# Kernel optimization log

Measured on AMD Instinct MI355X. Metric: run time of the kernel, lower is better.

The kernel has to match this reference:

```python
import jax, jax.numpy as jnp
import numpy as np

N = 100000   # nodes
E = 1600000  # edges (avg degree 16)
D = 48       # feature dim


def setup_inputs() -> dict:
    key = jax.random.key(0)
    k1, k2, k3, k4, k5 = jax.random.split(key, 5)
    src = jax.random.randint(k1, (E,), 0, N, dtype=jnp.int32)
    dst = jax.random.randint(k2, (E,), 0, N, dtype=jnp.int32)
    Y = jax.random.normal(k3, (N, D), dtype=jnp.float32)
    X = jax.random.normal(k4, (N, D), dtype=jnp.float32)
    w = jax.random.uniform(k5, (E,), dtype=jnp.float32)
    # graph.ndata['deg']: in-degree of each node
    deg = jax.ops.segment_sum(jnp.ones((E,), jnp.float32), dst, num_segments=N)
    alp = jnp.float32(0.5)   # step size alpha
    lam = jnp.float32(0.9)   # smoothing coefficient lambda
    return {"Y": Y, "X": X, "w": w, "deg": deg, "alp": alp, "lam": lam,
            "src": src, "dst": dst}


def reference(Y, X, w, deg, alp, lam, src, dst):
    n = Y.shape[0]

    def d_power_bias(Z, power):
        # (lam*D + (1-lam)*I)^power @ Z  -- diagonal rescale per node
        norm = jnp.power(lam * deg + (1.0 - lam), power)
        return Z * norm[:, None]

    # _prop: D^-1/2 A D^-1/2 with edge weights w (u_mul_e / sum SpMM)
    P = d_power_bias(Y, -0.5)
    msg = P[src] * w[:, None]                                  # [E, D] gather-mul
    AY = jax.ops.segment_sum(msg, dst, num_segments=n)         # scatter-add [N, D]
    AY = d_power_bias(AY, -0.5)

    return (1.0 - alp) * Y + alp * lam * AY + alp * d_power_bias(X, -1.0)
```

## Files before the change

kernel.cpp:

```cpp
#include <hip/hip_runtime.h>

typedef unsigned long long u64;
typedef unsigned short ushort8 __attribute__((ext_vector_type(8)));

#define NNODES 100000
#define NEDGES 1600000
#define DIM    48
#define QPN    12
#define GPN    6
#define YBF_STRIDE_US4 16
#define YBF_STRIDE_US8 8

#define NBUCK  1024
#define NPB    98
#define CELL_CAP 32
#define P1_NWG 250
#define P1_THREADS 1024
#define P1_GROUPS 1600
#define BUCKET_STRIDE (P1_NWG * CELL_CAP)

#define WS_BUCKETS_BYTES 1048576
#define WS_YBF_BYTES     (WS_BUCKETS_BYTES + (size_t)NBUCK * BUCKET_STRIDE * 8)


static __device__ __forceinline__ unsigned short f2bf(float f) {
    const unsigned u = __float_as_uint(f);
    const unsigned r = 0x7fffu + ((u >> 16) & 1u);
    return (unsigned short)((u + r) >> 16);
}

__global__ void __launch_bounds__(P1_THREADS) pass1_cells(
        const int* __restrict__ src, const int* __restrict__ dst,
        const float* __restrict__ w, const float* __restrict__ deg,
        const float* __restrict__ lam_p, const float* __restrict__ Y,
        int* __restrict__ cellcnt, u64* __restrict__ buckets,
        unsigned short* __restrict__ ybf) {
    __shared__ int lcnt[NBUCK];
    const int t = threadIdx.x;
    const int wg = blockIdx.x;
    const float lam = *lam_p;

    {
        const int stride = P1_NWG * P1_THREADS;
        for (int i = wg * P1_THREADS + t; i < NNODES * QPN; i += stride) {
            const int node = i / QPN;
            const int c = i - node * QPN;
            const float ns = rsqrtf(lam * deg[node] + (1.0f - lam));
            const float4 v = ((const float4*)Y)[i];
            ushort4 h;
            h.x = f2bf(v.x * ns); h.y = f2bf(v.y * ns);
            h.z = f2bf(v.z * ns); h.w = f2bf(v.w * ns);
            ((ushort4*)ybf)[node * YBF_STRIDE_US4 + c] = h;
        }
    }

    for (int b = t; b < NBUCK; b += P1_THREADS) lcnt[b] = 0;
    __syncthreads();

    const int gbase = wg * P1_GROUPS;
    for (int g = t; g < P1_GROUPS; g += P1_THREADS) {
        const int4   s4 = ((const int4*)src)[gbase + g];
        const int4   d4 = ((const int4*)dst)[gbase + g];
        const float4 w4 = ((const float4*)w)[gbase + g];
        const int   sv[4] = {s4.x, s4.y, s4.z, s4.w};
        const int   dv[4] = {d4.x, d4.y, d4.z, d4.w};
        const float wv[4] = {w4.x, w4.y, w4.z, w4.w};
        #pragma unroll
        for (int k = 0; k < 4; ++k) {
            const int b = (unsigned)dv[k] / NPB;
            const int dl = dv[k] - b * NPB;
            const int slot = atomicAdd(&lcnt[b], 1);
            if (slot < CELL_CAP) {
                const u64 payload = ((u64)__float_as_uint(wv[k]) << 32) |
                                    ((u64)(unsigned)sv[k] << 7) | (unsigned)dl;
                buckets[(size_t)b * BUCKET_STRIDE + wg * CELL_CAP + slot] = payload;
            }
        }
    }
    __syncthreads();

    for (int b = t; b < NBUCK; b += P1_THREADS)
        cellcnt[wg * NBUCK + b] = min(lcnt[b], CELL_CAP);
}

__global__ void __launch_bounds__(512) cell_sort_gather(
        const float* __restrict__ Y,
        const float* __restrict__ X,
        const float* __restrict__ deg,
        const float* __restrict__ alp_p,
        const float* __restrict__ lam_p,
        const int* __restrict__ cellcnt,
        const u64* __restrict__ buckets,
        const unsigned short* __restrict__ ybf,
        float* __restrict__ out) {
    __shared__ __align__(16) u64 raw[2048];
    __shared__ __align__(16) u64 srt[2048];
    __shared__ int ccnt[256];
    __shared__ int coff[256];
    __shared__ int hist[128];
    __shared__ int offl[128];
    __shared__ int cur[128];
    __shared__ int bcnt_sh;

    const int b = blockIdx.x;
    const int t = threadIdx.x;

    if (t < 256) ccnt[t] = (t < P1_NWG) ? cellcnt[t * NBUCK + b] : 0;
    __syncthreads();
    if (t < 256) coff[t] = ccnt[t];
    __syncthreads();
    for (int off = 1; off < 256; off <<= 1) {
        int v = 0;
        if (t < 256 && t >= off) v = coff[t - off];
        __syncthreads();
        if (t < 256) coff[t] += v;
        __syncthreads();
    }
    if (t == 255) bcnt_sh = coff[255];
    if (t < 256) coff[t] -= ccnt[t];
    if (t < 128) hist[t] = 0;
    __syncthreads();
    const int bcnt = bcnt_sh;

    if (t < 2 * P1_NWG) {
        const int c = t >> 1, par = t & 1;
        const int cnt = ccnt[c];
        const u64* cp = buckets + (size_t)b * BUCKET_STRIDE + c * CELL_CAP;
        const int o = coff[c];
        for (int j = par; j < cnt; j += 2) raw[o + j] = cp[j];
    }
    __syncthreads();

    for (int i = t; i < bcnt; i += 512)
        atomicAdd(&hist[(int)(raw[i] & 127u)], 1);
    __syncthreads();
    if (t < 128) offl[t] = hist[t];
    __syncthreads();
    for (int off = 1; off < 128; off <<= 1) {
        int v = 0;
        if (t < 128 && t >= off) v = offl[t - off];
        __syncthreads();
        if (t < 128) offl[t] += v;
        __syncthreads();
    }
    if (t < 128) {
        offl[t] -= hist[t];
        cur[t] = offl[t];
    }
    __syncthreads();
    for (int i = t; i < bcnt; i += 512) {
        const u64 p = raw[i];
        const int s2 = atomicAdd(&cur[(int)(p & 127u)], 1);
        srt[s2] = p;
    }
    __syncthreads();

    const float alp = *alp_p;
    const float lam = *lam_p;
    const float c0 = 1.0f - alp;
    const int node0 = b * NPB;
    for (int u = t; u < NPB * GPN; u += 512) {
        const int dl = u / GPN;
        const int q = u - dl * GPN;
        const int n = node0 + dl;
        if (n >= NNODES) break;
        const int st = offl[dl];
        const int len = hist[dl];
        float4 a0 = make_float4(0.f, 0.f, 0.f, 0.f);
        float4 a1 = make_float4(0.f, 0.f, 0.f, 0.f);
        #pragma unroll 4
        for (int j = 0; j < len; ++j) {
            const u64 p = srt[st + j];
            const unsigned s = (unsigned)(p >> 7) & 0x1ffffu;
            const float sc = __uint_as_float((unsigned)(p >> 32));
            const ushort8 h = ((const ushort8*)ybf)[(size_t)s * YBF_STRIDE_US8 + q];
            a0.x += __uint_as_float((unsigned)h[0] << 16) * sc;
            a0.y += __uint_as_float((unsigned)h[1] << 16) * sc;
            a0.z += __uint_as_float((unsigned)h[2] << 16) * sc;
            a0.w += __uint_as_float((unsigned)h[3] << 16) * sc;
            a1.x += __uint_as_float((unsigned)h[4] << 16) * sc;
            a1.y += __uint_as_float((unsigned)h[5] << 16) * sc;
            a1.z += __uint_as_float((unsigned)h[6] << 16) * sc;
            a1.w += __uint_as_float((unsigned)h[7] << 16) * sc;
        }
        const float ns = rsqrtf(lam * deg[n] + (1.0f - lam));
        const float ni = ns * ns;
        const float c1 = alp * lam * ns;
        const float c2 = alp * ni;
        const int f4 = (int)((size_t)n * QPN + q * 2);
        const float4 y0 = ((const float4*)Y)[f4];
        const float4 y1 = ((const float4*)Y)[f4 + 1];
        const float4 x0 = ((const float4*)X)[f4];
        const float4 x1 = ((const float4*)X)[f4 + 1];
        float4 r0, r1;
        r0.x = c0 * y0.x + c1 * a0.x + c2 * x0.x;
        r0.y = c0 * y0.y + c1 * a0.y + c2 * x0.y;
        r0.z = c0 * y0.z + c1 * a0.z + c2 * x0.z;
        r0.w = c0 * y0.w + c1 * a0.w + c2 * x0.w;
        r1.x = c0 * y1.x + c1 * a1.x + c2 * x1.x;
        r1.y = c0 * y1.y + c1 * a1.y + c2 * x1.y;
        r1.z = c0 * y1.z + c1 * a1.z + c2 * x1.z;
        r1.w = c0 * y1.w + c1 * a1.w + c2 * x1.w;
        ((float4*)out)[f4]     = r0;
        ((float4*)out)[f4 + 1] = r1;
    }
}

extern "C" void kernel_launch(void* const* d_in, const int* in_sizes, int n_in,
                              void* d_out, int out_size, void* d_ws, size_t ws_size,
                              hipStream_t stream) {
    const float* Y   = (const float*)d_in[0];
    const float* X   = (const float*)d_in[1];
    const float* w   = (const float*)d_in[2];
    const float* deg = (const float*)d_in[3];
    const float* alp = (const float*)d_in[4];
    const float* lam = (const float*)d_in[5];
    const int*   src = (const int*)d_in[6];
    const int*   dst = (const int*)d_in[7];
    float* out = (float*)d_out;

    int* cellcnt = (int*)d_ws;
    u64* buckets = (u64*)((char*)d_ws + WS_BUCKETS_BYTES);
    unsigned short* ybf = (unsigned short*)((char*)d_ws + WS_YBF_BYTES);

    pass1_cells<<<P1_NWG, P1_THREADS, 0, stream>>>(
        src, dst, w, deg, lam, Y, cellcnt, buckets, ybf);
    cell_sort_gather<<<NBUCK, 512, 0, stream>>>(
        Y, X, deg, alp, lam, cellcnt, buckets, ybf, out);
}
```

Baseline: 162.2 us.

## Balance edge gather across equal strips with LDS atomic accumulation and prefetch

The gather phase no longer gives each thread one destination node's variable-length edge list. The sorted edges of a bucket are split into 85 equal strips, each processed by six feature-chunk threads. Each thread accumulates runs of same-destination edges in registers and flushes them to an LDS float accumulator with atomics, with a two-deep software prefetch of the bf16 source rows. The shared-memory scans are also rewritten as wavefront shuffle scans, and the raw buffer is reused for the accumulator to keep LDS usage down. This targets load imbalance from uneven degrees and the barrier-heavy scans, at the cost of LDS atomics and nondeterministic summation order.

```diff
diff --git a/kernel.cpp b/kernel.cpp
--- a/kernel.cpp
+++ b/kernel.cpp
@@ -19,9 +19,10 @@
 #define P1_GROUPS 1600
 #define BUCKET_STRIDE (P1_NWG * CELL_CAP)
 
+#define NSTRIP 85
+
 #define WS_BUCKETS_BYTES 1048576
 #define WS_YBF_BYTES     (WS_BUCKETS_BYTES + (size_t)NBUCK * BUCKET_STRIDE * 8)
-
 
 static __device__ __forceinline__ unsigned short f2bf(float f) {
     const unsigned u = __float_as_uint(f);
@@ -93,31 +94,43 @@
         const u64* __restrict__ buckets,
         const unsigned short* __restrict__ ybf,
         float* __restrict__ out) {
-    __shared__ __align__(16) u64 raw[2048];
     __shared__ __align__(16) u64 srt[2048];
-    __shared__ int ccnt[256];
-    __shared__ int coff[256];
-    __shared__ int hist[128];
-    __shared__ int offl[128];
-    __shared__ int cur[128];
+    __shared__ __align__(16) char pool[19968];
+    __shared__ int wsum[4];
+    __shared__ int wsum2[2];
     __shared__ int bcnt_sh;
+
+    u64* raw   = (u64*)pool;
+    int* ccnt  = (int*)(pool + 16384);
+    int* coff  = ccnt + 256;
+    int* hist  = coff + 256;
+    int* cur   = hist + 128;
+    float* accum = (float*)pool;
 
     const int b = blockIdx.x;
     const int t = threadIdx.x;
 
-    if (t < 256) ccnt[t] = (t < P1_NWG) ? cellcnt[t * NBUCK + b] : 0;
-    __syncthreads();
-    if (t < 256) coff[t] = ccnt[t];
-    __syncthreads();
-    for (int off = 1; off < 256; off <<= 1) {
-        int v = 0;
-        if (t < 256 && t >= off) v = coff[t - off];
-        __syncthreads();
-        if (t < 256) coff[t] += v;
-        __syncthreads();
-    }
-    if (t == 255) bcnt_sh = coff[255];
-    if (t < 256) coff[t] -= ccnt[t];
+    if (t < 256) {
+        const int v = (t < P1_NWG) ? cellcnt[t * NBUCK + b] : 0;
+        ccnt[t] = v;
+        int s = v;
+        #pragma unroll
+        for (int d = 1; d < 64; d <<= 1) {
+            const int u2 = __shfl_up(s, d, 64);
+            if ((t & 63) >= d) s += u2;
+        }
+        if ((t & 63) == 63) wsum[t >> 6] = s;
+        coff[t] = s - v;
+    }
+    __syncthreads();
+    if (t < 256) {
+        const int w0 = t >> 6;
+        int add = 0;
+        #pragma unroll
+        for (int i = 0; i < 3; ++i) if (i < w0) add += wsum[i];
+        coff[t] += add;
+    }
+    if (t == 0) bcnt_sh = wsum[0] + wsum[1] + wsum[2] + wsum[3];
     if (t < 128) hist[t] = 0;
     __syncthreads();
     const int bcnt = bcnt_sh;
@@ -134,24 +147,79 @@
     for (int i = t; i < bcnt; i += 512)
         atomicAdd(&hist[(int)(raw[i] & 127u)], 1);
     __syncthreads();
-    if (t < 128) offl[t] = hist[t];
-    __syncthreads();
-    for (int off = 1; off < 128; off <<= 1) {
-        int v = 0;
-        if (t < 128 && t >= off) v = offl[t - off];
-        __syncthreads();
-        if (t < 128) offl[t] += v;
-        __syncthreads();
-    }
     if (t < 128) {
-        offl[t] -= hist[t];
-        cur[t] = offl[t];
-    }
+        const int v = hist[t];
+        int s = v;
+        #pragma unroll
+        for (int d = 1; d < 64; d <<= 1) {
+            const int u2 = __shfl_up(s, d, 64);
+            if ((t & 63) >= d) s += u2;
+        }
+        if ((t & 63) == 63) wsum2[t >> 6] = s;
+        cur[t] = s - v;
+    }
+    __syncthreads();
+    if (t >= 64 && t < 128) cur[t] += wsum2[0];
     __syncthreads();
     for (int i = t; i < bcnt; i += 512) {
         const u64 p = raw[i];
         const int s2 = atomicAdd(&cur[(int)(p & 127u)], 1);
         srt[s2] = p;
+    }
+    __syncthreads();
+
+    for (int i = t; i < NPB * DIM; i += 512) accum[i] = 0.0f;
+    __syncthreads();
+
+    if (t < NSTRIP * GPN) {
+        const int k = t / GPN;
+        const int q = t - k * GPN;
+        const int S = (bcnt + NSTRIP - 1) / NSTRIP;
+        const int e0 = k * S;
+        const int e1 = min(e0 + S, bcnt);
+        if (e0 < e1) {
+            float a[8];
+            #pragma unroll
+            for (int i = 0; i < 8; ++i) a[i] = 0.0f;
+            int curdl = -1;
+            int ea = e0;
+            int eb = min(e0 + 1, e1 - 1);
+            u64 p0 = srt[ea];
+            u64 p1 = srt[eb];
+            ushort8 h0 = ((const ushort8*)ybf)[
+                (size_t)((unsigned)(p0 >> 7) & 0x1ffffu) * YBF_STRIDE_US8 + q];
+            ushort8 h1 = ((const ushort8*)ybf)[
+                (size_t)((unsigned)(p1 >> 7) & 0x1ffffu) * YBF_STRIDE_US8 + q];
+            for (int e = e0; e < e1; ++e) {
+                const u64 p = p0;
+                const ushort8 h = h0;
+                p0 = p1; h0 = h1;
+                const int en = min(e + 2, e1 - 1);
+                p1 = srt[en];
+                h1 = ((const ushort8*)ybf)[
+                    (size_t)((unsigned)(p1 >> 7) & 0x1ffffu) * YBF_STRIDE_US8 + q];
+                const int dl = (int)(p & 127u);
+                if (dl != curdl) {
+                    if (curdl >= 0) {
+                        float* ap = accum + curdl * DIM + q * 8;
+                        #pragma unroll
+                        for (int i = 0; i < 8; ++i) atomicAdd(&ap[i], a[i]);
+                        #pragma unroll
+                        for (int i = 0; i < 8; ++i) a[i] = 0.0f;
+                    }
+                    curdl = dl;
+                }
+                const float sc = __uint_as_float((unsigned)(p >> 32));
+                #pragma unroll
+                for (int i = 0; i < 8; ++i)
+                    a[i] += __uint_as_float((unsigned)h[i] << 16) * sc;
+            }
+            if (curdl >= 0) {
+                float* ap = accum + curdl * DIM + q * 8;
+                #pragma unroll
+                for (int i = 0; i < 8; ++i) atomicAdd(&ap[i], a[i]);
+            }
+        }
     }
     __syncthreads();
 
@@ -164,25 +232,7 @@
         const int q = u - dl * GPN;
         const int n = node0 + dl;
         if (n >= NNODES) break;
-        const int st = offl[dl];
-        const int len = hist[dl];
-        float4 a0 = make_float4(0.f, 0.f, 0.f, 0.f);
-        float4 a1 = make_float4(0.f, 0.f, 0.f, 0.f);
-        #pragma unroll 4
-        for (int j = 0; j < len; ++j) {
-            const u64 p = srt[st + j];
-            const unsigned s = (unsigned)(p >> 7) & 0x1ffffu;
-            const float sc = __uint_as_float((unsigned)(p >> 32));
-            const ushort8 h = ((const ushort8*)ybf)[(size_t)s * YBF_STRIDE_US8 + q];
-            a0.x += __uint_as_float((unsigned)h[0] << 16) * sc;
-            a0.y += __uint_as_float((unsigned)h[1] << 16) * sc;
-            a0.z += __uint_as_float((unsigned)h[2] << 16) * sc;
-            a0.w += __uint_as_float((unsigned)h[3] << 16) * sc;
-            a1.x += __uint_as_float((unsigned)h[4] << 16) * sc;
-            a1.y += __uint_as_float((unsigned)h[5] << 16) * sc;
-            a1.z += __uint_as_float((unsigned)h[6] << 16) * sc;
-            a1.w += __uint_as_float((unsigned)h[7] << 16) * sc;
-        }
+        const float* ap = accum + dl * DIM + q * 8;
         const float ns = rsqrtf(lam * deg[n] + (1.0f - lam));
         const float ni = ns * ns;
         const float c1 = alp * lam * ns;
@@ -193,14 +243,14 @@
         const float4 x0 = ((const float4*)X)[f4];
         const float4 x1 = ((const float4*)X)[f4 + 1];
         float4 r0, r1;
-        r0.x = c0 * y0.x + c1 * a0.x + c2 * x0.x;
-        r0.y = c0 * y0.y + c1 * a0.y + c2 * x0.y;
-        r0.z = c0 * y0.z + c1 * a0.z + c2 * x0.z;
-        r0.w = c0 * y0.w + c1 * a0.w + c2 * x0.w;
-        r1.x = c0 * y1.x + c1 * a1.x + c2 * x1.x;
-        r1.y = c0 * y1.y + c1 * a1.y + c2 * x1.y;
-        r1.z = c0 * y1.z + c1 * a1.z + c2 * x1.z;
-        r1.w = c0 * y1.w + c1 * a1.w + c2 * x1.w;
+        r0.x = c0 * y0.x + c1 * ap[0] + c2 * x0.x;
+        r0.y = c0 * y0.y + c1 * ap[1] + c2 * x0.y;
+        r0.z = c0 * y0.z + c1 * ap[2] + c2 * x0.z;
+        r0.w = c0 * y0.w + c1 * ap[3] + c2 * x0.w;
+        r1.x = c0 * y1.x + c1 * ap[4] + c2 * x1.x;
+        r1.y = c0 * y1.y + c1 * ap[5] + c2 * x1.y;
+        r1.z = c0 * y1.z + c1 * ap[6] + c2 * x1.z;
+        r1.w = c0 * y1.w + c1 * ap[7] + c2 * x1.w;
         ((float4*)out)[f4]     = r0;
         ((float4*)out)[f4 + 1] = r1;
     }
```

After: 183.1 us. 1.13x slower.

## Use wavefront shuffle scans and degree-sorted node order in gather kernel

Applied to the files above, without the earlier changes.

Replaces the two shared-memory Hillis-Steele prefix scans (each with many __syncthreads) with wavefront __shfl_up scans plus a small cross-wave fixup, cutting barrier count. It also ranks the bucket's nodes by in-degree so that threads in a wavefront process nodes of similar length, reducing divergence in the gather loop. The ranking adds an O(NPB^2) shared-memory loop for 98 threads. The tail condition changes from break to continue to suit the permuted order.

```diff
diff --git a/kernel.cpp b/kernel.cpp
--- a/kernel.cpp
+++ b/kernel.cpp
@@ -21,7 +21,6 @@
 
 #define WS_BUCKETS_BYTES 1048576
 #define WS_YBF_BYTES     (WS_BUCKETS_BYTES + (size_t)NBUCK * BUCKET_STRIDE * 8)
-
 
 static __device__ __forceinline__ unsigned short f2bf(float f) {
     const unsigned u = __float_as_uint(f);
@@ -100,24 +99,35 @@
     __shared__ int hist[128];
     __shared__ int offl[128];
     __shared__ int cur[128];
+    __shared__ int sdl[NPB];
+    __shared__ int wsum[4];
+    __shared__ int wsum2[2];
     __shared__ int bcnt_sh;
 
     const int b = blockIdx.x;
     const int t = threadIdx.x;
 
-    if (t < 256) ccnt[t] = (t < P1_NWG) ? cellcnt[t * NBUCK + b] : 0;
-    __syncthreads();
-    if (t < 256) coff[t] = ccnt[t];
-    __syncthreads();
-    for (int off = 1; off < 256; off <<= 1) {
-        int v = 0;
-        if (t < 256 && t >= off) v = coff[t - off];
-        __syncthreads();
-        if (t < 256) coff[t] += v;
-        __syncthreads();
-    }
-    if (t == 255) bcnt_sh = coff[255];
-    if (t < 256) coff[t] -= ccnt[t];
+    if (t < 256) {
+        const int v = (t < P1_NWG) ? cellcnt[t * NBUCK + b] : 0;
+        ccnt[t] = v;
+        int s = v;
+        #pragma unroll
+        for (int d = 1; d < 64; d <<= 1) {
+            const int u2 = __shfl_up(s, d, 64);
+            if ((t & 63) >= d) s += u2;
+        }
+        if ((t & 63) == 63) wsum[t >> 6] = s;
+        coff[t] = s - v;
+    }
+    __syncthreads();
+    if (t < 256) {
+        const int w0 = t >> 6;
+        int add = 0;
+        #pragma unroll
+        for (int i = 0; i < 3; ++i) if (i < w0) add += wsum[i];
+        coff[t] += add;
+    }
+    if (t == 0) bcnt_sh = wsum[0] + wsum[1] + wsum[2] + wsum[3];
     if (t < 128) hist[t] = 0;
     __syncthreads();
     const int bcnt = bcnt_sh;
@@ -134,24 +144,36 @@
     for (int i = t; i < bcnt; i += 512)
         atomicAdd(&hist[(int)(raw[i] & 127u)], 1);
     __syncthreads();
-    if (t < 128) offl[t] = hist[t];
-    __syncthreads();
-    for (int off = 1; off < 128; off <<= 1) {
-        int v = 0;
-        if (t < 128 && t >= off) v = offl[t - off];
-        __syncthreads();
-        if (t < 128) offl[t] += v;
-        __syncthreads();
-    }
     if (t < 128) {
-        offl[t] -= hist[t];
-        cur[t] = offl[t];
-    }
+        const int v = hist[t];
+        int s = v;
+        #pragma unroll
+        for (int d = 1; d < 64; d <<= 1) {
+            const int u2 = __shfl_up(s, d, 64);
+            if ((t & 63) >= d) s += u2;
+        }
+        if ((t & 63) == 63) wsum2[t >> 6] = s;
+        offl[t] = s - v;
+    }
+    __syncthreads();
+    if (t >= 64 && t < 128) offl[t] += wsum2[0];
+    __syncthreads();
+    if (t < 128) cur[t] = offl[t];
     __syncthreads();
     for (int i = t; i < bcnt; i += 512) {
         const u64 p = raw[i];
         const int s2 = atomicAdd(&cur[(int)(p & 127u)], 1);
         srt[s2] = p;
+    }
+
+    if (t < NPB) {
+        const int len = hist[t];
+        int r = 0;
+        for (int j = 0; j < NPB; ++j) {
+            const int lj = hist[j];
+            r += (int)((lj > len) || (lj == len && j < t));
+        }
+        sdl[r] = t;
     }
     __syncthreads();
 
@@ -160,10 +182,11 @@
     const float c0 = 1.0f - alp;
     const int node0 = b * NPB;
     for (int u = t; u < NPB * GPN; u += 512) {
-        const int dl = u / GPN;
-        const int q = u - dl * GPN;
+        const int du = u / GPN;
+        const int q = u - du * GPN;
+        const int dl = sdl[du];
         const int n = node0 + dl;
-        if (n >= NNODES) break;
+        if (n >= NNODES) continue;
         const int st = offl[dl];
         const int len = hist[dl];
         float4 a0 = make_float4(0.f, 0.f, 0.f, 0.f);
```

After: 166.9 us. 1.03x slower.
